# Kernel tuning notes

Hardware: AMD Instinct MI355X
Metric: run time of the kernel (lower is better)

## Reference

```python
import jax, jax.numpy as jnp
import numpy as np

B, T, E, H, M2 = 8, 2048, 256, 2, 134
HD = E // H


def setup_inputs() -> dict:
    key = jax.random.key(0)
    ks = jax.random.split(key, 10)
    s = 0.02
    return {
        "X": jax.random.normal(ks[0], (B, T, E), dtype=jnp.float32),
        "Y": jax.random.uniform(ks[1], (B, M2), dtype=jnp.float32),
        "wpe": s * jax.random.normal(ks[2], (T, E), dtype=jnp.float32),
        "ln1_g": jnp.ones((E,), jnp.float32), "ln1_b": jnp.zeros((E,), jnp.float32),
        "attn_w": s * jax.random.normal(ks[3], (3 * E, E), dtype=jnp.float32),
        "attn_b": jnp.zeros((3 * E,), jnp.float32),
        "attnproj_w": s * jax.random.normal(ks[4], (E, E), dtype=jnp.float32),
        "attnproj_b": jnp.zeros((E,), jnp.float32),
        "ln2_g": jnp.ones((E,), jnp.float32), "ln2_b": jnp.zeros((E,), jnp.float32),
        "fc_w": s * jax.random.normal(ks[5], (2 * E, E), dtype=jnp.float32),
        "fc_b": jnp.zeros((2 * E,), jnp.float32),
        "mlpproj_w": s * jax.random.normal(ks[6], (E, 2 * E), dtype=jnp.float32),
        "mlpproj_b": jnp.zeros((E,), jnp.float32),
        "lnf_g": jnp.ones((E,), jnp.float32), "lnf_b": jnp.zeros((E,), jnp.float32),
        "head_w": s * jax.random.normal(ks[7], (M2, E), dtype=jnp.float32),
        "head_b": jnp.zeros((M2,), jnp.float32),
    }


def _ln(x, g, b, eps=1e-5):
    mu = x.mean(-1, keepdims=True)
    var = ((x - mu) ** 2).mean(-1, keepdims=True)
    return (x - mu) * jax.lax.rsqrt(var + eps) * g + b


def reference(X, Y, wpe, ln1_g, ln1_b, attn_w, attn_b, attnproj_w, attnproj_b,
              ln2_g, ln2_b, fc_w, fc_b, mlpproj_w, mlpproj_b, lnf_g, lnf_b,
              head_w, head_b):
    # positional ids = arange(T) -> wpe itself; cls ids = [0]*T/2 + [1]*T/2
    cls_ids = np.concatenate([np.zeros(T // 2, np.int32), np.ones(T // 2, np.int32)])
    x = X + wpe + wpe[cls_ids]                      # [B,T,E] (dropout = identity, eval)

    # single Block (n_layer=1), preceded by ReLU as in cross_mod loop
    x = jax.nn.relu(x)
    h = _ln(x, ln1_g, ln1_b)
    qkv = h @ attn_w.T + attn_b                     # [B,T,3E]
    q, k, v = jnp.split(qkv, 3, axis=-1)
    q, k, v = jax.nn.relu(q), jax.nn.relu(k), jax.nn.relu(v)
    split_heads = lambda t: t.reshape(B, T, H, HD).transpose(0, 2, 1, 3)
    q, k, v = split_heads(q), split_heads(k), split_heads(v)
    att = jnp.einsum('bhqd,bhkd->bhqk', q, k) * (1.0 / np.sqrt(HD))
    tril = jnp.tril(jnp.ones((T, T), dtype=bool))
    # masked_fill(-inf) then ReLU  ==  zero outside causal mask, ReLU inside
    att = jnp.where(tril, jax.nn.relu(att), 0.0)    # [B,H,T,T]
    y = jnp.einsum('bhqk,bhkd->bhqd', att, v)
    y = y.transpose(0, 2, 1, 3).reshape(B, T, E)
    x = x + (y @ attnproj_w.T + attnproj_b)

    h = _ln(x, ln2_g, ln2_b)
    x = x + (jax.nn.relu(h @ fc_w.T + fc_b) @ mlpproj_w.T + mlpproj_b)

    x = jax.nn.relu(x)
    x = _ln(x, lnf_g, lnf_b)
    x = jax.nn.relu(x)
    emb = x.mean(axis=1)                            # [B,E]
    logits = jax.nn.relu(emb @ head_w.T + head_b)   # [B,M2]

    loss1 = jnp.sqrt(jnp.mean((logits - Y) ** 2))
    e1, e2 = emb[:, : E // 2], emb[:, E // 2:]
    loss3 = jnp.sqrt(jnp.mean((e1 - e2) ** 2))
    loss = 50.0 * loss1 + loss3
    return (e1, e2, loss, loss1, loss3, logits)
```

## Files before the change

### kernel.cpp

```cpp
#include <hip/hip_runtime.h>
#include <hip/hip_bf16.h>

#define Bc 8
#define Tc 2048
#define Ec 256
#define Hc 2
#define HDc 128
#define Mrows (Bc*Tc)
#define M2c 134

using bfx8  = __attribute__((ext_vector_type(8))) __bf16;
using f32x4 = __attribute__((ext_vector_type(4))) float;

__device__ __forceinline__ void gll16(const __bf16* g, __bf16* lds) {
    __builtin_amdgcn_global_load_lds(
        (const __attribute__((address_space(1))) unsigned int*)g,
        (__attribute__((address_space(3))) unsigned int*)lds, 16, 0, 0);
}

__global__ __launch_bounds__(256) void embed_prep_k(const float* X, const float* wpe,
                                                    const float* g, const float* bb,
                                                    const float* attn_w, const float* apw,
                                                    const float* fcw, const float* mpw,
                                                    __bf16* wb, float* embsum,
                                                    __bf16* xres, __bf16* hb) {
    int m = blockIdx.x;
    int e = threadIdx.x;
    if (m < 2048) {
        int i = m * 256 + e;
        if (i < 196608)       wb[i] = (__bf16)attn_w[i];
        else if (i < 262144)  wb[i] = (__bf16)apw[i - 196608];
        else if (i < 393216)  wb[i] = (__bf16)fcw[i - 262144];
        else                  wb[i] = (__bf16)mpw[i - 393216];
        if (m < 8) embsum[m * 256 + e] = 0.f;
    }
    int t = m & (Tc - 1);
    float v = X[(size_t)m * Ec + e] + wpe[(size_t)t * Ec + e] + wpe[(size_t)(t >= 1024) * Ec + e];
    v = fmaxf(v, 0.f);
    xres[(size_t)m * Ec + e] = (__bf16)v;
    float s1 = v, s2 = v * v;
    #pragma unroll
    for (int o = 32; o; o >>= 1) { s1 += __shfl_xor(s1, o, 64); s2 += __shfl_xor(s2, o, 64); }
    __shared__ float a1[4], a2[4];
    int w = threadIdx.x >> 6;
    if ((threadIdx.x & 63) == 0) { a1[w] = s1; a2[w] = s2; }
    __syncthreads();
    float m1 = (a1[0] + a1[1] + a1[2] + a1[3]) * (1.f / 256.f);
    float m2 = (a2[0] + a2[1] + a2[2] + a2[3]) * (1.f / 256.f);
    float r = rsqrtf(m2 - m1 * m1 + 1e-5f);
    hb[(size_t)m * Ec + e] = (__bf16)((v - m1) * r * g[e] + bb[e]);
}

__global__ __launch_bounds__(256) void gemm_qkv(const __bf16* __restrict__ A,
                                                const __bf16* __restrict__ Bw,
                                                const float* __restrict__ bias,
                                                __bf16* __restrict__ Qb,
                                                __bf16* __restrict__ Kb,
                                                __bf16* __restrict__ Vb) {
    const int K = 256;
    __shared__ __bf16 As[128 * 64];
    __shared__ __bf16 Bs[128 * 64];
    const int tid = threadIdx.x, w = tid >> 6, l = tid & 63;
    const int m0 = blockIdx.y * 128, n0 = blockIdx.x * 128;
    const int wr = w >> 1, wc = w & 1;
    const int quad = l >> 4, col15 = l & 15;

    f32x4 acc[4][4];
    f32x4 zz = {0.f, 0.f, 0.f, 0.f};
    #pragma unroll
    for (int i = 0; i < 4; i++)
        #pragma unroll
        for (int j = 0; j < 4; j++) acc[i][j] = zz;

    const int lrow = l >> 3;
    const int pbs  = l & 7;

    for (int kb = 0; kb < K; kb += 64) {
        #pragma unroll
        for (int it = 0; it < 4; it++) {
            int chunk = w * 4 + it;
            int row = chunk * 8 + lrow;
            int lb = pbs ^ (row & 7);
            gll16(A  + (size_t)(m0 + row) * K + kb + lb * 8, As + chunk * 512);
            gll16(Bw + (size_t)(n0 + row) * K + kb + lb * 8, Bs + chunk * 512);
        }
        __syncthreads();
        #pragma unroll
        for (int ks = 0; ks < 2; ks++) {
            bfx8 af[4], bfr[4];
            #pragma unroll
            for (int rt = 0; rt < 4; rt++) {
                int row = wr * 64 + rt * 16 + col15;
                int pb = (ks * 4 + quad) ^ (row & 7);
                af[rt] = *(const bfx8*)(As + row * 64 + pb * 8);
            }
            #pragma unroll
            for (int ct = 0; ct < 4; ct++) {
                int row = wc * 64 + ct * 16 + col15;
                int pb = (ks * 4 + quad) ^ (row & 7);
                bfr[ct] = *(const bfx8*)(Bs + row * 64 + pb * 8);
            }
            #pragma unroll
            for (int rt = 0; rt < 4; rt++)
                #pragma unroll
                for (int ct = 0; ct < 4; ct++)
                    acc[rt][ct] = __builtin_amdgcn_mfma_f32_16x16x32_bf16(af[rt], bfr[ct], acc[rt][ct], 0, 0, 0);
        }
        __syncthreads();
    }

    #pragma unroll
    for (int rt = 0; rt < 4; rt++)
        #pragma unroll
        for (int ct = 0; ct < 4; ct++) {
            int mgb = m0 + wr * 64 + rt * 16 + quad * 4;
            int ng  = n0 + wc * 64 + ct * 16 + col15;
            float bsv = bias[ng];
            #pragma unroll
            for (int r = 0; r < 4; r++) {
                float val = fmaxf(acc[rt][ct][r] + bsv, 0.f);
                int mg = mgb + r;
                int sel = ng >> 8;
                int hh = (ng >> 7) & 1;
                int d = ng & 127;
                int bb = mg >> 11, tt = mg & (Tc - 1);
                size_t idx = ((size_t)((bb * 2 + hh) * Tc + tt)) * HDc + d;
                __bf16 bv = (__bf16)val;
                if (sel == 0) Qb[idx] = bv;
                else if (sel == 1) Kb[idx] = bv;
                else Vb[idx] = bv;
            }
        }
}

__global__ __launch_bounds__(256) void transpose_v(const unsigned short* Vb, unsigned short* Vt) {
    __shared__ unsigned short tile[64][66];
    int kt = blockIdx.x, dt = blockIdx.y, bh = blockIdx.z;
    int tid = threadIdx.x;
    int k0 = kt * 64, d0 = dt * 64;
    int rr = tid >> 4, cc = (tid & 15) * 4;
    #pragma unroll
    for (int p = 0; p < 4; p++) {
        int k = p * 16 + rr;
        const unsigned short* src = Vb + ((size_t)(bh * Tc + k0 + k)) * HDc + d0 + cc;
        ushort4 vv = *(const ushort4*)src;
        tile[k][cc] = vv.x; tile[k][cc + 1] = vv.y; tile[k][cc + 2] = vv.z; tile[k][cc + 3] = vv.w;
    }
    __syncthreads();
    #pragma unroll
    for (int p = 0; p < 4; p++) {
        int d = p * 16 + rr;
        unsigned short* dst = Vt + ((size_t)(bh * HDc + d0 + d)) * Tc + k0 + cc;
        ushort4 ov;
        ov.x = tile[cc][d]; ov.y = tile[cc + 1][d]; ov.z = tile[cc + 2][d]; ov.w = tile[cc + 3][d];
        *(ushort4*)dst = ov;
    }
}

__global__ __launch_bounds__(256, 4) void attn6_k(const __bf16* __restrict__ Qb,
                                                  const __bf16* __restrict__ Kb,
                                                  const __bf16* __restrict__ Vt,
                                                  __bf16* __restrict__ Y1,
                                                  __bf16* __restrict__ Y2,
                                                  __bf16* __restrict__ Y3,
                                                  __bf16* __restrict__ Y4) {
    __shared__ __bf16 Ks[64 * 128];
    __shared__ __bf16 Vs[128 * 64];
    __shared__ __bf16 Ss[64 * 64];
    int bid = blockIdx.x;
    int lane8 = bid & 7;
    int s = bid >> 3;
    int bh = ((s & 1) << 3) | lane8;
    int f = s >> 1;
    int qt, ch;
    if (f < 8)       { qt = f;                    ch = 0; }
    else if (f < 24) { qt = 8 + ((f - 8) >> 1);   ch = (f - 8) & 1; }
    else if (f < 48) { int r = f - 24; int d3 = r / 3; qt = 16 + d3; ch = r - 3 * d3; }
    else             { int r = f - 48; qt = 24 + (r >> 2); ch = r & 3; }
    int Q0 = qt * 64;
    int kts = ch * 8;
    int kte = min(kts + 8, qt + 1);

    int tid = threadIdx.x, w = tid >> 6, l = tid & 63;
    int quad = l >> 4, col15 = l & 15;
    const int lrowK = l >> 4, pbsK = l & 15;
    const int lrowV = l >> 3, pbsV = l & 7;

    #pragma unroll
    for (int it = 0; it < 4; it++) {
        int chunk = w * 4 + it;
        int row = chunk * 4 + lrowK;
        int lb = pbsK ^ (row & 7);
        gll16(Qb + ((size_t)(bh * Tc + Q0 + row)) * HDc + lb * 8, Ks + chunk * 512);
    }
    __syncthreads();
    bfx8 qf[4];
    #pragma unroll
    for (int ks = 0; ks < 4; ks++) {
        int row = w * 16 + col15;
        int pb = (ks * 4 + quad) ^ (row & 7);
        qf[ks] = *(const bfx8*)(Ks + row * 128 + pb * 8);
    }

    f32x4 zz = {0.f, 0.f, 0.f, 0.f};
    f32x4 yacc[8];
    #pragma unroll
    for (int i = 0; i < 8; i++) yacc[i] = zz;

    for (int kt = kts; kt < kte; kt++) {
        __syncthreads();
        #pragma unroll
        for (int it = 0; it < 4; it++) {
            int chunk = w * 4 + it;
            int rowK = chunk * 4 + lrowK;
            int lbK = pbsK ^ (rowK & 7);
            gll16(Kb + ((size_t)(bh * Tc + kt * 64 + rowK)) * HDc + lbK * 8, Ks + chunk * 512);
            int rowV = chunk * 8 + lrowV;
            int lbV = pbsV ^ (rowV & 7);
            gll16(Vt + ((size_t)(bh * HDc + rowV)) * Tc + kt * 64 + lbV * 8, Vs + chunk * 512);
        }
        __syncthreads();

        f32x4 sacc[4];
        #pragma unroll
        for (int i = 0; i < 4; i++) sacc[i] = zz;
        #pragma unroll
        for (int ks = 0; ks < 4; ks++) {
            #pragma unroll
            for (int ct = 0; ct < 4; ct++) {
                int row = ct * 16 + col15;
                int pb = (ks * 4 + quad) ^ (row & 7);
                bfx8 kf = *(const bfx8*)(Ks + row * 128 + pb * 8);
                sacc[ct] = __builtin_amdgcn_mfma_f32_16x16x32_bf16(qf[ks], kf, sacc[ct], 0, 0, 0);
            }
        }

        #pragma unroll
        for (int ct = 0; ct < 4; ct++) {
            int kl = ct * 16 + col15;
            int kg = kt * 64 + kl;
            int blk = kl >> 3, off = kl & 7;
            #pragma unroll
            for (int r = 0; r < 4; r++) {
                int qlw = w * 16 + quad * 4 + r;
                float val = (kg <= Q0 + qlw) ? fmaxf(sacc[ct][r], 0.f) : 0.f;
                int pb = blk ^ (qlw & 7);
                Ss[qlw * 64 + pb * 8 + off] = (__bf16)val;
            }
        }

        #pragma unroll
        for (int ks = 0; ks < 2; ks++) {
            int rowS = w * 16 + col15;
            int pbS = (ks * 4 + quad) ^ (rowS & 7);
            bfx8 sf = *(const bfx8*)(Ss + rowS * 64 + pbS * 8);
            #pragma unroll
            for (int dt = 0; dt < 8; dt++) {
                int row = dt * 16 + col15;
                int pb = (ks * 4 + quad) ^ (row & 7);
                bfx8 vf = *(const bfx8*)(Vs + row * 64 + pb * 8);
                yacc[dt] = __builtin_amdgcn_mfma_f32_16x16x32_bf16(sf, vf, yacc[dt], 0, 0, 0);
            }
        }
    }

    __bf16* Yp = (ch == 0) ? Y1 : (ch == 1) ? Y2 : (ch == 2) ? Y3 : Y4;
    int b = bh >> 1, h = bh & 1;
    const float sc = 0.08838834764831845f;
    #pragma unroll
    for (int dt = 0; dt < 8; dt++) {
        int d = dt * 16 + col15;
        #pragma unroll
        for (int r = 0; r < 4; r++) {
            int q = Q0 + w * 16 + quad * 4 + r;
            Yp[((size_t)(b * Tc + q)) * Ec + h * HDc + d] = (__bf16)(yacc[dt][r] * sc);
        }
    }
}

__global__ __launch_bounds__(256, 1) void mega_k(const __bf16* __restrict__ Y1,
                                                 const __bf16* __restrict__ Y2,
                                                 const __bf16* __restrict__ Y3,
                                                 const __bf16* __restrict__ Y4,
                                                 const __bf16* __restrict__ wap,
                                                 const float* __restrict__ apb,
                                                 const __bf16* __restrict__ xres,
                                                 const float* __restrict__ ln2_g,
                                                 const float* __restrict__ ln2_b,
                                                 const __bf16* __restrict__ wfc,
                                                 const float* __restrict__ fcb,
                                                 const __bf16* __restrict__ wmp,
                                                 const float* __restrict__ mpb,
                                                 const float* __restrict__ lnf_g,
                                                 const float* __restrict__ lnf_b,
                                                 float* __restrict__ embsum) {
    __shared__ __bf16 h2s[4 * 4096];
    __shared__ __bf16 fc64[8 * 4096];
    __shared__ __bf16 Bs[256 * 64];
    __shared__ float cs[256];
    const int tid = threadIdx.x, w = tid >> 6, l = tid & 63;
    const int m0 = blockIdx.x * 64;
    const int quad = l >> 4, col15 = l & 15;
    const int lrow = l >> 3, pbs = l & 7;
    f32x4 zz = {0.f, 0.f, 0.f, 0.f};
    cs[tid] = 0.f;

    int nsum = (((m0 & (Tc - 1)) >> 6) + 8) >> 3;
    const __bf16* Ys[4] = {Y1, Y2, Y3, Y4};
    __bf16* As = fc64;

    f32x4 acc[16];
    #pragma unroll
    for (int i = 0; i < 16; i++) acc[i] = zz;

    for (int kb = 0; kb < 256; kb += 64) {
        bfx8 av[2]; int rows[2], blks[2];
        #pragma unroll
        for (int it = 0; it < 2; it++) {
            int idx = it * 256 + tid;
            int row = idx >> 3, blk = idx & 7;
            rows[it] = row; blks[it] = blk;
            size_t off = (size_t)(m0 + row) * 256 + kb + blk * 8;
            bfx8 a1 = *(const bfx8*)(Y1 + off);
            float tmp[8];
            #pragma unroll
            for (int jj = 0; jj < 8; jj++) tmp[jj] = (float)a1[jj];
            for (int j = 1; j < nsum; j++) {
                bfx8 aj = *(const bfx8*)(Ys[j] + off);
                #pragma unroll
                for (int jj = 0; jj < 8; jj++) tmp[jj] += (float)aj[jj];
            }
            #pragma unroll
            for (int jj = 0; jj < 8; jj++) a1[jj] = (__bf16)tmp[jj];
            av[it] = a1;
        }
        __syncthreads();
        #pragma unroll
        for (int it = 0; it < 2; it++) {
            int row = rows[it];
            int pb = blks[it] ^ (row & 7);
            *(bfx8*)(As + row * 64 + pb * 8) = av[it];
        }
        #pragma unroll
        for (int it = 0; it < 8; it++) {
            int chunk = w * 8 + it;
            int row = chunk * 8 + lrow;
            int lb = pbs ^ (row & 7);
            gll16(wap + (size_t)row * 256 + kb + lb * 8, Bs + chunk * 512);
        }
        __syncthreads();
        #pragma unroll
        for (int ks = 0; ks < 2; ks++) {
            int arow = w * 16 + col15;
            int apbk = (ks * 4 + quad) ^ (arow & 7);
            bfx8 af = *(const bfx8*)(As + arow * 64 + apbk * 8);
            #pragma unroll
            for (int ct = 0; ct < 16; ct++) {
                int brow = ct * 16 + col15;
                int bpb = (ks * 4 + quad) ^ (brow & 7);
                bfx8 bf = *(const bfx8*)(Bs + brow * 64 + bpb * 8);
                acc[ct] = __builtin_amdgcn_mfma_f32_16x16x32_bf16(af, bf, acc[ct], 0, 0, 0);
            }
        }
    }

    float xv[16][4];
    #pragma unroll
    for (int ct = 0; ct < 16; ct++) {
        int ng = ct * 16 + col15;
        float bsv = apb[ng];
        #pragma unroll
        for (int r = 0; r < 4; r++) {
            int mg = m0 + w * 16 + quad * 4 + r;
            xv[ct][r] = acc[ct][r] + bsv + (float)xres[(size_t)mg * 256 + ng];
        }
    }
    {
        float s1[4], s2[4];
        #pragma unroll
        for (int r = 0; r < 4; r++) {
            float a = 0.f, b2 = 0.f;
            #pragma unroll
            for (int ct = 0; ct < 16; ct++) { a += xv[ct][r]; b2 += xv[ct][r] * xv[ct][r]; }
            #pragma unroll
            for (int o = 1; o < 16; o <<= 1) { a += __shfl_xor(a, o, 64); b2 += __shfl_xor(b2, o, 64); }
            s1[r] = a; s2[r] = b2;
        }
        #pragma unroll
        for (int r = 0; r < 4; r++) {
            float mu = s1[r] * (1.f / 256.f);
            float var = s2[r] * (1.f / 256.f) - mu * mu;
            float rs = rsqrtf(var + 1e-5f);
            int row = w * 16 + quad * 4 + r;
            #pragma unroll
            for (int ct = 0; ct < 16; ct++) {
                int ng = ct * 16 + col15;
                float h = (xv[ct][r] - mu) * rs * ln2_g[ng] + ln2_b[ng];
                int panel = ng >> 6, c = ng & 63;
                h2s[panel * 4096 + row * 64 + ((c >> 3) ^ (row & 7)) * 8 + (c & 7)] = (__bf16)h;
            }
        }
    }

    for (int half = 0; half < 2; half++) {
        f32x4 acc2[16];
        #pragma unroll
        for (int i = 0; i < 16; i++) acc2[i] = zz;
        for (int kb = 0; kb < 256; kb += 64) {
            __syncthreads();
            #pragma unroll
            for (int it = 0; it < 8; it++) {
                int chunk = w * 8 + it;
                int row = chunk * 8 + lrow;
                int lb = pbs ^ (row & 7);
                gll16(wfc + (size_t)(half * 256 + row) * 256 + kb + lb * 8, Bs + chunk * 512);
            }
            __syncthreads();
            int panel = kb >> 6;
            #pragma unroll
            for (int ks = 0; ks < 2; ks++) {
                int arow = w * 16 + col15;
                int apbk = (ks * 4 + quad) ^ (arow & 7);
                bfx8 af = *(const bfx8*)(h2s + panel * 4096 + arow * 64 + apbk * 8);
                #pragma unroll
                for (int ct = 0; ct < 16; ct++) {
                    int brow = ct * 16 + col15;
                    int bpb = (ks * 4 + quad) ^ (brow & 7);
                    bfx8 bf = *(const bfx8*)(Bs + brow * 64 + bpb * 8);
                    acc2[ct] = __builtin_amdgcn_mfma_f32_16x16x32_bf16(af, bf, acc2[ct], 0, 0, 0);
                }
            }
        }
        #pragma unroll
        for (int ct = 0; ct < 16; ct++) {
            int col = half * 256 + ct * 16 + col15;
            float bsv = fcb[col];
            int panel = col >> 6, c = col & 63;
            #pragma unroll
            for (int r = 0; r < 4; r++) {
                int row = w * 16 + quad * 4 + r;
                float val = fmaxf(acc2[ct][r] + bsv, 0.f);
                fc64[panel * 4096 + row * 64 + ((c >> 3) ^ (row & 7)) * 8 + (c & 7)] = (__bf16)val;
            }
        }
    }

    #pragma unroll
    for (int i = 0; i < 16; i++) acc[i] = zz;
    for (int kb = 0; kb < 512; kb += 64) {
        __syncthreads();
        #pragma unroll
        for (int it = 0; it < 8; it++) {
            int chunk = w * 8 + it;
            int row = chunk * 8 + lrow;
            int lb = pbs ^ (row & 7);
            gll16(wmp + (size_t)row * 512 + kb + lb * 8, Bs + chunk * 512);
        }
        __syncthreads();
        int panel = kb >> 6;
        #pragma unroll
        for (int ks = 0; ks < 2; ks++) {
            int arow = w * 16 + col15;
            int apbk = (ks * 4 + quad) ^ (arow & 7);
            bfx8 af = *(const bfx8*)(fc64 + panel * 4096 + arow * 64 + apbk * 8);
            #pragma unroll
            for (int ct = 0; ct < 16; ct++) {
                int brow = ct * 16 + col15;
                int bpb = (ks * 4 + quad) ^ (brow & 7);
                bfx8 bf = *(const bfx8*)(Bs + brow * 64 + bpb * 8);
                acc[ct] = __builtin_amdgcn_mfma_f32_16x16x32_bf16(af, bf, acc[ct], 0, 0, 0);
            }
        }
    }

    #pragma unroll
    for (int ct = 0; ct < 16; ct++) {
        int ng = ct * 16 + col15;
        float bsv = mpb[ng];
        #pragma unroll
        for (int r = 0; r < 4; r++)
            xv[ct][r] = fmaxf(acc[ct][r] + bsv + xv[ct][r], 0.f);
    }
    float s1[4], s2[4];
    #pragma unroll
    for (int r = 0; r < 4; r++) {
        float a = 0.f, b2 = 0.f;
        #pragma unroll
        for (int ct = 0; ct < 16; ct++) { a += xv[ct][r]; b2 += xv[ct][r] * xv[ct][r]; }
        #pragma unroll
        for (int o = 1; o < 16; o <<= 1) { a += __shfl_xor(a, o, 64); b2 += __shfl_xor(b2, o, 64); }
        s1[r] = a; s2[r] = b2;
    }
    float colsum[16];
    #pragma unroll
    for (int ct = 0; ct < 16; ct++) colsum[ct] = 0.f;
    #pragma unroll
    for (int r = 0; r < 4; r++) {
        float mu = s1[r] * (1.f / 256.f);
        float var = s2[r] * (1.f / 256.f) - mu * mu;
        float rs = rsqrtf(var + 1e-5f);
        #pragma unroll
        for (int ct = 0; ct < 16; ct++) {
            int ng = ct * 16 + col15;
            float h = (xv[ct][r] - mu) * rs * lnf_g[ng] + lnf_b[ng];
            colsum[ct] += fmaxf(h, 0.f);
        }
    }
    #pragma unroll
    for (int ct = 0; ct < 16; ct++) {
        colsum[ct] += __shfl_xor(colsum[ct], 16, 64);
        colsum[ct] += __shfl_xor(colsum[ct], 32, 64);
    }
    if (quad == 0) {
        #pragma unroll
        for (int ct = 0; ct < 16; ct++)
            atomicAdd(&cs[ct * 16 + col15], colsum[ct]);
    }
    __syncthreads();
    atomicAdd(&embsum[(m0 >> 11) * 256 + tid], cs[tid]);
}

__global__ __launch_bounds__(256) void final_k(const float* embsum, const float* Yt,
                                               const float* head_w, const float* head_b,
                                               float* out) {
    __shared__ float semb[2048];
    __shared__ float slog[1072];
    int tid = threadIdx.x;
    for (int i = tid; i < 2048; i += 256) semb[i] = embsum[i] * (1.f / 2048.f);
    __syncthreads();
    float part1 = 0.f;
    for (int idx = tid; idx < 1072; idx += 256) {
        int b = idx / M2c, n = idx - b * M2c;
        float acc = head_b[n];
        const float* wn = head_w + (size_t)n * Ec;
        const float* e = semb + b * Ec;
        #pragma unroll 8
        for (int k = 0; k < Ec; k++) acc += e[k] * wn[k];
        acc = fmaxf(acc, 0.f);
        slog[idx] = acc;
        float d = acc - Yt[idx];
        part1 += d * d;
    }
    float part3 = 0.f;
    for (int idx = tid; idx < 1024; idx += 256) {
        int b = idx >> 7, i = idx & 127;
        float d = semb[b * Ec + i] - semb[b * Ec + 128 + i];
        part3 += d * d;
    }
    #pragma unroll
    for (int o = 32; o; o >>= 1) { part1 += __shfl_xor(part1, o, 64); part3 += __shfl_xor(part3, o, 64); }
    __shared__ float r1[4], r3[4];
    int w = tid >> 6;
    if ((tid & 63) == 0) { r1[w] = part1; r3[w] = part3; }
    __syncthreads();
    float l1 = sqrtf((r1[0] + r1[1] + r1[2] + r1[3]) / 1072.f);
    float l3 = sqrtf((r3[0] + r3[1] + r3[2] + r3[3]) / 1024.f);
    for (int idx = tid; idx < 1024; idx += 256) {
        int b = idx >> 7, i = idx & 127;
        out[idx]        = semb[b * Ec + i];
        out[1024 + idx] = semb[b * Ec + 128 + i];
    }
    if (tid == 0) {
        out[2048] = 50.f * l1 + l3;
        out[2049] = l1;
        out[2050] = l3;
    }
    for (int idx = tid; idx < 1072; idx += 256) out[2051 + idx] = slog[idx];
}

extern "C" void kernel_launch(void* const* d_in, const int* in_sizes, int n_in,
                              void* d_out, int out_size, void* d_ws, size_t ws_size,
                              hipStream_t stream) {
    const float* X        = (const float*)d_in[0];
    const float* Yt       = (const float*)d_in[1];
    const float* wpe      = (const float*)d_in[2];
    const float* ln1_g    = (const float*)d_in[3];
    const float* ln1_b    = (const float*)d_in[4];
    const float* attn_w   = (const float*)d_in[5];
    const float* attn_b   = (const float*)d_in[6];
    const float* apw      = (const float*)d_in[7];
    const float* apb      = (const float*)d_in[8];
    const float* ln2_g    = (const float*)d_in[9];
    const float* ln2_b    = (const float*)d_in[10];
    const float* fcw      = (const float*)d_in[11];
    const float* fcb      = (const float*)d_in[12];
    const float* mpw      = (const float*)d_in[13];
    const float* mpb      = (const float*)d_in[14];
    const float* lnf_g    = (const float*)d_in[15];
    const float* lnf_b    = (const float*)d_in[16];
    const float* head_w   = (const float*)d_in[17];
    const float* head_b   = (const float*)d_in[18];

    char* ws = (char*)d_ws;
    const size_t MB = 1048576;
    __bf16* xres   = (__bf16*)(ws + 0 * MB);
    __bf16* hb     = (__bf16*)(ws + 8 * MB);
    __bf16* Qb     = (__bf16*)(ws + 16 * MB);
    __bf16* Kb     = (__bf16*)(ws + 24 * MB);
    __bf16* Vb     = (__bf16*)(ws + 32 * MB);
    __bf16* Vt     = (__bf16*)(ws + 40 * MB);
    __bf16* Y1     = (__bf16*)(ws + 48 * MB);
    __bf16* Y2     = (__bf16*)(ws + 56 * MB);
    __bf16* wb     = (__bf16*)(ws + 64 * MB);
    float*  embsum = (float*)(ws + 65 * MB);

    __bf16* Y3 = hb;
    __bf16* Y4 = Vb;

    __bf16* wqkv = wb;
    __bf16* wap  = wb + 196608;
    __bf16* wfc  = wb + 262144;
    __bf16* wmp  = wb + 393216;

    embed_prep_k<<<Mrows, 256, 0, stream>>>(X, wpe, ln1_g, ln1_b,
                                            attn_w, apw, fcw, mpw, wb, embsum, xres, hb);
    gemm_qkv<<<dim3(6, 128), 256, 0, stream>>>(hb, wqkv, attn_b, Qb, Kb, Vb);
    transpose_v<<<dim3(32, 2, 16), 256, 0, stream>>>((const unsigned short*)Vb, (unsigned short*)Vt);
    attn6_k<<<1280, 256, 0, stream>>>(Qb, Kb, Vt, Y1, Y2, Y3, Y4);
    mega_k<<<256, 256, 0, stream>>>(Y1, Y2, Y3, Y4, wap, apb, xres, ln2_g, ln2_b,
                                    wfc, fcb, wmp, mpb, lnf_g, lnf_b, embsum);
    final_k<<<1, 256, 0, stream>>>(embsum, Yt, head_w, head_b, (float*)d_out);
}
```

Before: 250.4 us.

## Fuse V transpose into QKV GEMM epilogue and pair causal query tiles in attention

The QKV GEMM now writes V already transposed via an LDS staging tile, so the separate transpose kernel and its extra global round trip are gone. The attention kernel pairs query tile p with tile 31-p so every block gets equal causal work split into four chunks, sharing each K/V tile load between both query tiles. The mega kernel now always sums all four partial outputs. In exchange, attention uses more registers and LDS (occupancy hint lowered to 3) and the GEMM gains a 34KB transpose buffer, which may lower its occupancy.

```diff
diff --git a/kernel.cpp b/kernel.cpp
--- a/kernel.cpp
+++ b/kernel.cpp
@@ -56,14 +56,16 @@
                                                 const float* __restrict__ bias,
                                                 __bf16* __restrict__ Qb,
                                                 __bf16* __restrict__ Kb,
-                                                __bf16* __restrict__ Vb) {
+                                                unsigned short* __restrict__ Vt) {
     const int K = 256;
     __shared__ __bf16 As[128 * 64];
     __shared__ __bf16 Bs[128 * 64];
+    __shared__ unsigned short trans[128][136];
     const int tid = threadIdx.x, w = tid >> 6, l = tid & 63;
     const int m0 = blockIdx.y * 128, n0 = blockIdx.x * 128;
     const int wr = w >> 1, wc = w & 1;
     const int quad = l >> 4, col15 = l & 15;
+    const int isV = (n0 >= 512);
 
     f32x4 acc[4][4];
     f32x4 zz = {0.f, 0.f, 0.f, 0.f};
@@ -113,51 +115,43 @@
     for (int rt = 0; rt < 4; rt++)
         #pragma unroll
         for (int ct = 0; ct < 4; ct++) {
-            int mgb = m0 + wr * 64 + rt * 16 + quad * 4;
             int ng  = n0 + wc * 64 + ct * 16 + col15;
             float bsv = bias[ng];
             #pragma unroll
             for (int r = 0; r < 4; r++) {
+                int mg = m0 + wr * 64 + rt * 16 + quad * 4 + r;
                 float val = fmaxf(acc[rt][ct][r] + bsv, 0.f);
-                int mg = mgb + r;
-                int sel = ng >> 8;
-                int hh = (ng >> 7) & 1;
-                int d = ng & 127;
-                int bb = mg >> 11, tt = mg & (Tc - 1);
-                size_t idx = ((size_t)((bb * 2 + hh) * Tc + tt)) * HDc + d;
                 __bf16 bv = (__bf16)val;
-                if (sel == 0) Qb[idx] = bv;
-                else if (sel == 1) Kb[idx] = bv;
-                else Vb[idx] = bv;
-            }
-        }
+                if (isV) {
+                    int d = ng & 127;
+                    int tl = mg - m0;
+                    trans[d][tl] = *(unsigned short*)&bv;
+                } else {
+                    int sel = ng >> 8;
+                    int hh = (ng >> 7) & 1;
+                    int d = ng & 127;
+                    int bb = mg >> 11, tt = mg & (Tc - 1);
+                    size_t idx = ((size_t)((bb * 2 + hh) * Tc + tt)) * HDc + d;
+                    if (sel == 0) Qb[idx] = bv;
+                    else Kb[idx] = bv;
+                }
+            }
+        }
+    if (isV) {
+        __syncthreads();
+        int h = (n0 >> 7) & 1;
+        int b = m0 >> 11, t0 = m0 & (Tc - 1);
+        int bh = b * 2 + h;
+        int d = tid >> 1, th = tid & 1;
+        unsigned short* dst = Vt + ((size_t)(bh * HDc + d)) * Tc + t0 + th * 64;
+        const unsigned short* src = &trans[d][th * 64];
+        #pragma unroll
+        for (int i = 0; i < 8; i++)
+            *(uint4*)(dst + i * 8) = *(const uint4*)(src + i * 8);
+    }
 }
 
-__global__ __launch_bounds__(256) void transpose_v(const unsigned short* Vb, unsigned short* Vt) {
-    __shared__ unsigned short tile[64][66];
-    int kt = blockIdx.x, dt = blockIdx.y, bh = blockIdx.z;
-    int tid = threadIdx.x;
-    int k0 = kt * 64, d0 = dt * 64;
-    int rr = tid >> 4, cc = (tid & 15) * 4;
-    #pragma unroll
-    for (int p = 0; p < 4; p++) {
-        int k = p * 16 + rr;
-        const unsigned short* src = Vb + ((size_t)(bh * Tc + k0 + k)) * HDc + d0 + cc;
-        ushort4 vv = *(const ushort4*)src;
-        tile[k][cc] = vv.x; tile[k][cc + 1] = vv.y; tile[k][cc + 2] = vv.z; tile[k][cc + 3] = vv.w;
-    }
-    __syncthreads();
-    #pragma unroll
-    for (int p = 0; p < 4; p++) {
-        int d = p * 16 + rr;
-        unsigned short* dst = Vt + ((size_t)(bh * HDc + d0 + d)) * Tc + k0 + cc;
-        ushort4 ov;
-        ov.x = tile[cc][d]; ov.y = tile[cc + 1][d]; ov.z = tile[cc + 2][d]; ov.w = tile[cc + 3][d];
-        *(ushort4*)dst = ov;
-    }
-}
-
-__global__ __launch_bounds__(256, 4) void attn6_k(const __bf16* __restrict__ Qb,
+__global__ __launch_bounds__(256, 3) void attn7_k(const __bf16* __restrict__ Qb,
                                                   const __bf16* __restrict__ Kb,
                                                   const __bf16* __restrict__ Vt,
                                                   __bf16* __restrict__ Y1,
@@ -166,48 +160,69 @@
                                                   __bf16* __restrict__ Y4) {
     __shared__ __bf16 Ks[64 * 128];
     __shared__ __bf16 Vs[128 * 64];
-    __shared__ __bf16 Ss[64 * 64];
+    __shared__ __bf16 SsA[64 * 64];
+    __shared__ __bf16 SsB[64 * 64];
     int bid = blockIdx.x;
     int lane8 = bid & 7;
     int s = bid >> 3;
     int bh = ((s & 1) << 3) | lane8;
     int f = s >> 1;
-    int qt, ch;
-    if (f < 8)       { qt = f;                    ch = 0; }
-    else if (f < 24) { qt = 8 + ((f - 8) >> 1);   ch = (f - 8) & 1; }
-    else if (f < 48) { int r = f - 24; int d3 = r / 3; qt = 16 + d3; ch = r - 3 * d3; }
-    else             { int r = f - 48; qt = 24 + (r >> 2); ch = r & 3; }
-    int Q0 = qt * 64;
-    int kts = ch * 8;
-    int kte = min(kts + 8, qt + 1);
+    int p = f >> 2, ch = f & 3;
+    int Q0A = p * 64, Q0B = (31 - p) * 64;
+    const int offs[5] = {0, 9, 17, 25, 33};
+    int u0 = offs[ch], u1 = offs[ch + 1];
+    int twoP = 2 * (p + 1);
 
     int tid = threadIdx.x, w = tid >> 6, l = tid & 63;
     int quad = l >> 4, col15 = l & 15;
     const int lrowK = l >> 4, pbsK = l & 15;
     const int lrowV = l >> 3, pbsV = l & 7;
 
+    bfx8 qfA[4], qfB[4];
     #pragma unroll
     for (int it = 0; it < 4; it++) {
         int chunk = w * 4 + it;
         int row = chunk * 4 + lrowK;
         int lb = pbsK ^ (row & 7);
-        gll16(Qb + ((size_t)(bh * Tc + Q0 + row)) * HDc + lb * 8, Ks + chunk * 512);
+        gll16(Qb + ((size_t)(bh * Tc + Q0A + row)) * HDc + lb * 8, Ks + chunk * 512);
     }
     __syncthreads();
-    bfx8 qf[4];
     #pragma unroll
     for (int ks = 0; ks < 4; ks++) {
         int row = w * 16 + col15;
         int pb = (ks * 4 + quad) ^ (row & 7);
-        qf[ks] = *(const bfx8*)(Ks + row * 128 + pb * 8);
+        qfA[ks] = *(const bfx8*)(Ks + row * 128 + pb * 8);
+    }
+    __syncthreads();
+    #pragma unroll
+    for (int it = 0; it < 4; it++) {
+        int chunk = w * 4 + it;
+        int row = chunk * 4 + lrowK;
+        int lb = pbsK ^ (row & 7);
+        gll16(Qb + ((size_t)(bh * Tc + Q0B + row)) * HDc + lb * 8, Ks + chunk * 512);
+    }
+    __syncthreads();
+    #pragma unroll
+    for (int ks = 0; ks < 4; ks++) {
+        int row = w * 16 + col15;
+        int pb = (ks * 4 + quad) ^ (row & 7);
+        qfB[ks] = *(const bfx8*)(Ks + row * 128 + pb * 8);
     }
 
     f32x4 zz = {0.f, 0.f, 0.f, 0.f};
-    f32x4 yacc[8];
-    #pragma unroll
-    for (int i = 0; i < 8; i++) yacc[i] = zz;
-
-    for (int kt = kts; kt < kte; kt++) {
+    f32x4 yaccA[8], yaccB[8];
+    #pragma unroll
+    for (int i = 0; i < 8; i++) { yaccA[i] = zz; yaccB[i] = zz; }
+
+    int u = u0;
+    while (u < u1) {
+        int kt, hasA, hasB;
+        if (u < twoP) {
+            kt = u >> 1;
+            if ((u & 1) == 0) { hasA = 1; hasB = (u + 1 < u1) ? 1 : 0; u += 1 + hasB; }
+            else              { hasA = 0; hasB = 1; u += 1; }
+        } else { kt = u - p - 1; hasA = 0; hasB = 1; u += 1; }
+
         __syncthreads();
         #pragma unroll
         for (int it = 0; it < 4; it++) {
@@ -221,17 +236,27 @@
         }
         __syncthreads();
 
-        f32x4 sacc[4];
-        #pragma unroll
-        for (int i = 0; i < 4; i++) sacc[i] = zz;
+        f32x4 sA[4], sB[4];
+        #pragma unroll
+        for (int i = 0; i < 4; i++) { sA[i] = zz; sB[i] = zz; }
         #pragma unroll
         for (int ks = 0; ks < 4; ks++) {
+            bfx8 kf[4];
             #pragma unroll
             for (int ct = 0; ct < 4; ct++) {
                 int row = ct * 16 + col15;
                 int pb = (ks * 4 + quad) ^ (row & 7);
-                bfx8 kf = *(const bfx8*)(Ks + row * 128 + pb * 8);
-                sacc[ct] = __builtin_amdgcn_mfma_f32_16x16x32_bf16(qf[ks], kf, sacc[ct], 0, 0, 0);
+                kf[ct] = *(const bfx8*)(Ks + row * 128 + pb * 8);
+            }
+            if (hasB) {
+                #pragma unroll
+                for (int ct = 0; ct < 4; ct++)
+                    sB[ct] = __builtin_amdgcn_mfma_f32_16x16x32_bf16(qfB[ks], kf[ct], sB[ct], 0, 0, 0);
+            }
+            if (hasA) {
+                #pragma unroll
+                for (int ct = 0; ct < 4; ct++)
+                    sA[ct] = __builtin_amdgcn_mfma_f32_16x16x32_bf16(qfA[ks], kf[ct], sA[ct], 0, 0, 0);
             }
         }
 
@@ -243,9 +268,15 @@
             #pragma unroll
             for (int r = 0; r < 4; r++) {
                 int qlw = w * 16 + quad * 4 + r;
-                float val = (kg <= Q0 + qlw) ? fmaxf(sacc[ct][r], 0.f) : 0.f;
                 int pb = blk ^ (qlw & 7);
-                Ss[qlw * 64 + pb * 8 + off] = (__bf16)val;
+                if (hasB) {
+                    float vB = (kg <= Q0B + qlw) ? fmaxf(sB[ct][r], 0.f) : 0.f;
+                    SsB[qlw * 64 + pb * 8 + off] = (__bf16)vB;
+                }
+                if (hasA) {
+                    float vA = (kg <= Q0A + qlw) ? fmaxf(sA[ct][r], 0.f) : 0.f;
+                    SsA[qlw * 64 + pb * 8 + off] = (__bf16)vA;
+                }
             }
         }
 
@@ -253,13 +284,16 @@
         for (int ks = 0; ks < 2; ks++) {
             int rowS = w * 16 + col15;
             int pbS = (ks * 4 + quad) ^ (rowS & 7);
-            bfx8 sf = *(const bfx8*)(Ss + rowS * 64 + pbS * 8);
+            bfx8 sfB, sfA;
+            if (hasB) sfB = *(const bfx8*)(SsB + rowS * 64 + pbS * 8);
+            if (hasA) sfA = *(const bfx8*)(SsA + rowS * 64 + pbS * 8);
             #pragma unroll
             for (int dt = 0; dt < 8; dt++) {
                 int row = dt * 16 + col15;
                 int pb = (ks * 4 + quad) ^ (row & 7);
                 bfx8 vf = *(const bfx8*)(Vs + row * 64 + pb * 8);
-                yacc[dt] = __builtin_amdgcn_mfma_f32_16x16x32_bf16(sf, vf, yacc[dt], 0, 0, 0);
+                if (hasB) yaccB[dt] = __builtin_amdgcn_mfma_f32_16x16x32_bf16(sfB, vf, yaccB[dt], 0, 0, 0);
+                if (hasA) yaccA[dt] = __builtin_amdgcn_mfma_f32_16x16x32_bf16(sfA, vf, yaccA[dt], 0, 0, 0);
             }
         }
     }
@@ -272,8 +306,10 @@
         int d = dt * 16 + col15;
         #pragma unroll
         for (int r = 0; r < 4; r++) {
-            int q = Q0 + w * 16 + quad * 4 + r;
-            Yp[((size_t)(b * Tc + q)) * Ec + h * HDc + d] = (__bf16)(yacc[dt][r] * sc);
+            int qa = Q0A + w * 16 + quad * 4 + r;
+            int qb2 = Q0B + w * 16 + quad * 4 + r;
+            Yp[((size_t)(b * Tc + qa)) * Ec + h * HDc + d] = (__bf16)(yaccA[dt][r] * sc);
+            Yp[((size_t)(b * Tc + qb2)) * Ec + h * HDc + d] = (__bf16)(yaccB[dt][r] * sc);
         }
     }
 }
@@ -304,9 +340,6 @@
     const int lrow = l >> 3, pbs = l & 7;
     f32x4 zz = {0.f, 0.f, 0.f, 0.f};
     cs[tid] = 0.f;
-
-    int nsum = (((m0 & (Tc - 1)) >> 6) + 8) >> 3;
-    const __bf16* Ys[4] = {Y1, Y2, Y3, Y4};
     __bf16* As = fc64;
 
     f32x4 acc[16];
@@ -322,16 +355,12 @@
             rows[it] = row; blks[it] = blk;
             size_t off = (size_t)(m0 + row) * 256 + kb + blk * 8;
             bfx8 a1 = *(const bfx8*)(Y1 + off);
-            float tmp[8];
-            #pragma unroll
-            for (int jj = 0; jj < 8; jj++) tmp[jj] = (float)a1[jj];
-            for (int j = 1; j < nsum; j++) {
-                bfx8 aj = *(const bfx8*)(Ys[j] + off);
-                #pragma unroll
-                for (int jj = 0; jj < 8; jj++) tmp[jj] += (float)aj[jj];
-            }
-            #pragma unroll
-            for (int jj = 0; jj < 8; jj++) a1[jj] = (__bf16)tmp[jj];
+            bfx8 a2 = *(const bfx8*)(Y2 + off);
+            bfx8 a3 = *(const bfx8*)(Y3 + off);
+            bfx8 a4 = *(const bfx8*)(Y4 + off);
+            #pragma unroll
+            for (int jj = 0; jj < 8; jj++)
+                a1[jj] = (__bf16)(((float)a1[jj] + (float)a2[jj]) + ((float)a3[jj] + (float)a4[jj]));
             av[it] = a1;
         }
         __syncthreads();
@@ -614,9 +643,8 @@
 
     embed_prep_k<<<Mrows, 256, 0, stream>>>(X, wpe, ln1_g, ln1_b,
                                             attn_w, apw, fcw, mpw, wb, embsum, xres, hb);
-    gemm_qkv<<<dim3(6, 128), 256, 0, stream>>>(hb, wqkv, attn_b, Qb, Kb, Vb);
-    transpose_v<<<dim3(32, 2, 16), 256, 0, stream>>>((const unsigned short*)Vb, (unsigned short*)Vt);
-    attn6_k<<<1280, 256, 0, stream>>>(Qb, Kb, Vt, Y1, Y2, Y3, Y4);
+    gemm_qkv<<<dim3(6, 128), 256, 0, stream>>>(hb, wqkv, attn_b, Qb, Kb, (unsigned short*)Vt);
+    attn7_k<<<1024, 256, 0, stream>>>(Qb, Kb, Vt, Y1, Y2, Y3, Y4);
     mega_k<<<256, 256, 0, stream>>>(Y1, Y2, Y3, Y4, wap, apb, xres, ln2_g, ln2_b,
                                     wfc, fcb, wmp, mpb, lnf_g, lnf_b, embsum);
     final_k<<<1, 256, 0, stream>>>(embsum, Yt, head_w, head_b, (float*)d_out);
```

Result: slower. 373.9 us (+49.3%).

## Fuse V transpose into QKV GEMM epilogue and use 128-row query tiles

Applied to the files above, without the earlier changes.

The QKV GEMM now writes V directly in transposed layout through an LDS staging tile, which removes the separate transpose kernel and its extra round trip through global memory. The attention kernel moves from 64-row to 128-row query tiles, with each wave handling two 16-row subtiles. This reuses each K/V tile load across twice as many queries and halves the grid. The costs are more registers and LDS per block (occupancy hint lowered from 4 to 3) and a larger LDS footprint in the GEMM. The chunk-count formula in mega_k is updated to match the new split.

```diff
diff --git a/kernel.cpp b/kernel.cpp
--- a/kernel.cpp
+++ b/kernel.cpp
@@ -56,14 +56,16 @@
                                                 const float* __restrict__ bias,
                                                 __bf16* __restrict__ Qb,
                                                 __bf16* __restrict__ Kb,
-                                                __bf16* __restrict__ Vb) {
+                                                unsigned short* __restrict__ Vt) {
     const int K = 256;
     __shared__ __bf16 As[128 * 64];
     __shared__ __bf16 Bs[128 * 64];
+    __shared__ unsigned short trans[128][136];
     const int tid = threadIdx.x, w = tid >> 6, l = tid & 63;
     const int m0 = blockIdx.y * 128, n0 = blockIdx.x * 128;
     const int wr = w >> 1, wc = w & 1;
     const int quad = l >> 4, col15 = l & 15;
+    const int isV = (n0 >= 512);
 
     f32x4 acc[4][4];
     f32x4 zz = {0.f, 0.f, 0.f, 0.f};
@@ -113,73 +115,66 @@
     for (int rt = 0; rt < 4; rt++)
         #pragma unroll
         for (int ct = 0; ct < 4; ct++) {
-            int mgb = m0 + wr * 64 + rt * 16 + quad * 4;
             int ng  = n0 + wc * 64 + ct * 16 + col15;
             float bsv = bias[ng];
             #pragma unroll
             for (int r = 0; r < 4; r++) {
+                int mg = m0 + wr * 64 + rt * 16 + quad * 4 + r;
                 float val = fmaxf(acc[rt][ct][r] + bsv, 0.f);
-                int mg = mgb + r;
-                int sel = ng >> 8;
-                int hh = (ng >> 7) & 1;
-                int d = ng & 127;
-                int bb = mg >> 11, tt = mg & (Tc - 1);
-                size_t idx = ((size_t)((bb * 2 + hh) * Tc + tt)) * HDc + d;
                 __bf16 bv = (__bf16)val;
-                if (sel == 0) Qb[idx] = bv;
-                else if (sel == 1) Kb[idx] = bv;
-                else Vb[idx] = bv;
-            }
-        }
+                if (isV) {
+                    int d = ng & 127;
+                    int tl = mg - m0;
+                    trans[d][tl] = *(unsigned short*)&bv;
+                } else {
+                    int sel = ng >> 8;
+                    int hh = (ng >> 7) & 1;
+                    int d = ng & 127;
+                    int bb = mg >> 11, tt = mg & (Tc - 1);
+                    size_t idx = ((size_t)((bb * 2 + hh) * Tc + tt)) * HDc + d;
+                    if (sel == 0) Qb[idx] = bv;
+                    else Kb[idx] = bv;
+                }
+            }
+        }
+    if (isV) {
+        __syncthreads();
+        int h = (n0 >> 7) & 1;
+        int b = m0 >> 11, t0 = m0 & (Tc - 1);
+        int bh = b * 2 + h;
+        int d = tid >> 1, th = tid & 1;
+        unsigned short* dst = Vt + ((size_t)(bh * HDc + d)) * Tc + t0 + th * 64;
+        const unsigned short* src = &trans[d][th * 64];
+        #pragma unroll
+        for (int i = 0; i < 8; i++)
+            *(uint4*)(dst + i * 8) = *(const uint4*)(src + i * 8);
+    }
 }
 
-__global__ __launch_bounds__(256) void transpose_v(const unsigned short* Vb, unsigned short* Vt) {
-    __shared__ unsigned short tile[64][66];
-    int kt = blockIdx.x, dt = blockIdx.y, bh = blockIdx.z;
-    int tid = threadIdx.x;
-    int k0 = kt * 64, d0 = dt * 64;
-    int rr = tid >> 4, cc = (tid & 15) * 4;
-    #pragma unroll
-    for (int p = 0; p < 4; p++) {
-        int k = p * 16 + rr;
-        const unsigned short* src = Vb + ((size_t)(bh * Tc + k0 + k)) * HDc + d0 + cc;
-        ushort4 vv = *(const ushort4*)src;
-        tile[k][cc] = vv.x; tile[k][cc + 1] = vv.y; tile[k][cc + 2] = vv.z; tile[k][cc + 3] = vv.w;
-    }
-    __syncthreads();
-    #pragma unroll
-    for (int p = 0; p < 4; p++) {
-        int d = p * 16 + rr;
-        unsigned short* dst = Vt + ((size_t)(bh * HDc + d0 + d)) * Tc + k0 + cc;
-        ushort4 ov;
-        ov.x = tile[cc][d]; ov.y = tile[cc + 1][d]; ov.z = tile[cc + 2][d]; ov.w = tile[cc + 3][d];
-        *(ushort4*)dst = ov;
-    }
-}
-
-__global__ __launch_bounds__(256, 4) void attn6_k(const __bf16* __restrict__ Qb,
+__global__ __launch_bounds__(256, 3) void attn8_k(const __bf16* __restrict__ Qb,
                                                   const __bf16* __restrict__ Kb,
                                                   const __bf16* __restrict__ Vt,
                                                   __bf16* __restrict__ Y1,
                                                   __bf16* __restrict__ Y2,
                                                   __bf16* __restrict__ Y3,
                                                   __bf16* __restrict__ Y4) {
-    __shared__ __bf16 Ks[64 * 128];
-    __shared__ __bf16 Vs[128 * 64];
-    __shared__ __bf16 Ss[64 * 64];
+    __shared__ __bf16 smem[3 * 8192];
+    __bf16* Ks = smem;
+    __bf16* Vs = smem + 8192;
+    __bf16* Ss = smem + 16384;
     int bid = blockIdx.x;
     int lane8 = bid & 7;
     int s = bid >> 3;
     int bh = ((s & 1) << 3) | lane8;
     int f = s >> 1;
     int qt, ch;
-    if (f < 8)       { qt = f;                    ch = 0; }
-    else if (f < 24) { qt = 8 + ((f - 8) >> 1);   ch = (f - 8) & 1; }
-    else if (f < 48) { int r = f - 24; int d3 = r / 3; qt = 16 + d3; ch = r - 3 * d3; }
-    else             { int r = f - 48; qt = 24 + (r >> 2); ch = r & 3; }
-    int Q0 = qt * 64;
+    if (f < 4)       { qt = f;                   ch = 0; }
+    else if (f < 12) { qt = 4 + ((f - 4) >> 1);  ch = (f - 4) & 1; }
+    else if (f < 24) { int r = f - 12; int d3 = r / 3; qt = 8 + d3; ch = r - 3 * d3; }
+    else             { int r = f - 24; qt = 12 + (r >> 2); ch = r & 3; }
+    int Q0 = qt * 128;
     int kts = ch * 8;
-    int kte = min(kts + 8, qt + 1);
+    int kte = min(kts + 8, 2 * qt + 2);
 
     int tid = threadIdx.x, w = tid >> 6, l = tid & 63;
     int quad = l >> 4, col15 = l & 15;
@@ -187,25 +182,29 @@
     const int lrowV = l >> 3, pbsV = l & 7;
 
     #pragma unroll
-    for (int it = 0; it < 4; it++) {
-        int chunk = w * 4 + it;
+    for (int it = 0; it < 8; it++) {
+        int chunk = w * 8 + it;
         int row = chunk * 4 + lrowK;
         int lb = pbsK ^ (row & 7);
-        gll16(Qb + ((size_t)(bh * Tc + Q0 + row)) * HDc + lb * 8, Ks + chunk * 512);
+        gll16(Qb + ((size_t)(bh * Tc + Q0 + row)) * HDc + lb * 8, smem + chunk * 512);
     }
     __syncthreads();
-    bfx8 qf[4];
-    #pragma unroll
-    for (int ks = 0; ks < 4; ks++) {
-        int row = w * 16 + col15;
-        int pb = (ks * 4 + quad) ^ (row & 7);
-        qf[ks] = *(const bfx8*)(Ks + row * 128 + pb * 8);
-    }
+    bfx8 qf[2][4];
+    #pragma unroll
+    for (int rt = 0; rt < 2; rt++)
+        #pragma unroll
+        for (int ks = 0; ks < 4; ks++) {
+            int row = w * 32 + rt * 16 + col15;
+            int pb = (ks * 4 + quad) ^ (row & 7);
+            qf[rt][ks] = *(const bfx8*)(smem + row * 128 + pb * 8);
+        }
 
     f32x4 zz = {0.f, 0.f, 0.f, 0.f};
-    f32x4 yacc[8];
-    #pragma unroll
-    for (int i = 0; i < 8; i++) yacc[i] = zz;
+    f32x4 yacc[2][8];
+    #pragma unroll
+    for (int rt = 0; rt < 2; rt++)
+        #pragma unroll
+        for (int i = 0; i < 8; i++) yacc[rt][i] = zz;
 
     for (int kt = kts; kt < kte; kt++) {
         __syncthreads();
@@ -221,45 +220,60 @@
         }
         __syncthreads();
 
-        f32x4 sacc[4];
-        #pragma unroll
-        for (int i = 0; i < 4; i++) sacc[i] = zz;
+        f32x4 sacc[2][4];
+        #pragma unroll
+        for (int rt = 0; rt < 2; rt++)
+            #pragma unroll
+            for (int i = 0; i < 4; i++) sacc[rt][i] = zz;
         #pragma unroll
         for (int ks = 0; ks < 4; ks++) {
+            bfx8 kf[4];
             #pragma unroll
             for (int ct = 0; ct < 4; ct++) {
                 int row = ct * 16 + col15;
                 int pb = (ks * 4 + quad) ^ (row & 7);
-                bfx8 kf = *(const bfx8*)(Ks + row * 128 + pb * 8);
-                sacc[ct] = __builtin_amdgcn_mfma_f32_16x16x32_bf16(qf[ks], kf, sacc[ct], 0, 0, 0);
-            }
-        }
-
-        #pragma unroll
-        for (int ct = 0; ct < 4; ct++) {
-            int kl = ct * 16 + col15;
-            int kg = kt * 64 + kl;
-            int blk = kl >> 3, off = kl & 7;
-            #pragma unroll
-            for (int r = 0; r < 4; r++) {
-                int qlw = w * 16 + quad * 4 + r;
-                float val = (kg <= Q0 + qlw) ? fmaxf(sacc[ct][r], 0.f) : 0.f;
-                int pb = blk ^ (qlw & 7);
-                Ss[qlw * 64 + pb * 8 + off] = (__bf16)val;
-            }
-        }
+                kf[ct] = *(const bfx8*)(Ks + row * 128 + pb * 8);
+            }
+            #pragma unroll
+            for (int rt = 0; rt < 2; rt++)
+                #pragma unroll
+                for (int ct = 0; ct < 4; ct++)
+                    sacc[rt][ct] = __builtin_amdgcn_mfma_f32_16x16x32_bf16(qf[rt][ks], kf[ct], sacc[rt][ct], 0, 0, 0);
+        }
+
+        #pragma unroll
+        for (int rt = 0; rt < 2; rt++)
+            #pragma unroll
+            for (int ct = 0; ct < 4; ct++) {
+                int kl = ct * 16 + col15;
+                int kg = kt * 64 + kl;
+                int blk = kl >> 3, off = kl & 7;
+                #pragma unroll
+                for (int r = 0; r < 4; r++) {
+                    int qlw = w * 32 + rt * 16 + quad * 4 + r;
+                    float val = (kg <= Q0 + qlw) ? fmaxf(sacc[rt][ct][r], 0.f) : 0.f;
+                    int pb = blk ^ (qlw & 7);
+                    Ss[qlw * 64 + pb * 8 + off] = (__bf16)val;
+                }
+            }
 
         #pragma unroll
         for (int ks = 0; ks < 2; ks++) {
-            int rowS = w * 16 + col15;
-            int pbS = (ks * 4 + quad) ^ (rowS & 7);
-            bfx8 sf = *(const bfx8*)(Ss + rowS * 64 + pbS * 8);
+            bfx8 sf[2];
+            #pragma unroll
+            for (int rt = 0; rt < 2; rt++) {
+                int rowS = w * 32 + rt * 16 + col15;
+                int pbS = (ks * 4 + quad) ^ (rowS & 7);
+                sf[rt] = *(const bfx8*)(Ss + rowS * 64 + pbS * 8);
+            }
             #pragma unroll
             for (int dt = 0; dt < 8; dt++) {
                 int row = dt * 16 + col15;
                 int pb = (ks * 4 + quad) ^ (row & 7);
                 bfx8 vf = *(const bfx8*)(Vs + row * 64 + pb * 8);
-                yacc[dt] = __builtin_amdgcn_mfma_f32_16x16x32_bf16(sf, vf, yacc[dt], 0, 0, 0);
+                #pragma unroll
+                for (int rt = 0; rt < 2; rt++)
+                    yacc[rt][dt] = __builtin_amdgcn_mfma_f32_16x16x32_bf16(sf[rt], vf, yacc[rt][dt], 0, 0, 0);
             }
         }
     }
@@ -268,14 +282,16 @@
     int b = bh >> 1, h = bh & 1;
     const float sc = 0.08838834764831845f;
     #pragma unroll
-    for (int dt = 0; dt < 8; dt++) {
-        int d = dt * 16 + col15;
-        #pragma unroll
-        for (int r = 0; r < 4; r++) {
-            int q = Q0 + w * 16 + quad * 4 + r;
-            Yp[((size_t)(b * Tc + q)) * Ec + h * HDc + d] = (__bf16)(yacc[dt][r] * sc);
-        }
-    }
+    for (int rt = 0; rt < 2; rt++)
+        #pragma unroll
+        for (int dt = 0; dt < 8; dt++) {
+            int d = dt * 16 + col15;
+            #pragma unroll
+            for (int r = 0; r < 4; r++) {
+                int q = Q0 + w * 32 + rt * 16 + quad * 4 + r;
+                Yp[((size_t)(b * Tc + q)) * Ec + h * HDc + d] = (__bf16)(yacc[rt][dt][r] * sc);
+            }
+        }
 }
 
 __global__ __launch_bounds__(256, 1) void mega_k(const __bf16* __restrict__ Y1,
@@ -304,10 +320,11 @@
     const int lrow = l >> 3, pbs = l & 7;
     f32x4 zz = {0.f, 0.f, 0.f, 0.f};
     cs[tid] = 0.f;
-
-    int nsum = (((m0 & (Tc - 1)) >> 6) + 8) >> 3;
+    __bf16* As = fc64;
+
+    int qt128 = (m0 & (Tc - 1)) >> 7;
+    int nsum = (2 * qt128 + 9) >> 3;
     const __bf16* Ys[4] = {Y1, Y2, Y3, Y4};
-    __bf16* As = fc64;
 
     f32x4 acc[16];
     #pragma unroll
@@ -614,9 +631,8 @@
 
     embed_prep_k<<<Mrows, 256, 0, stream>>>(X, wpe, ln1_g, ln1_b,
                                             attn_w, apw, fcw, mpw, wb, embsum, xres, hb);
-    gemm_qkv<<<dim3(6, 128), 256, 0, stream>>>(hb, wqkv, attn_b, Qb, Kb, Vb);
-    transpose_v<<<dim3(32, 2, 16), 256, 0, stream>>>((const unsigned short*)Vb, (unsigned short*)Vt);
-    attn6_k<<<1280, 256, 0, stream>>>(Qb, Kb, Vt, Y1, Y2, Y3, Y4);
+    gemm_qkv<<<dim3(6, 128), 256, 0, stream>>>(hb, wqkv, attn_b, Qb, Kb, (unsigned short*)Vt);
+    attn8_k<<<640, 256, 0, stream>>>(Qb, Kb, Vt, Y1, Y2, Y3, Y4);
     mega_k<<<256, 256, 0, stream>>>(Y1, Y2, Y3, Y4, wap, apb, xres, ln2_g, ln2_b,
                                     wfc, fcb, wmp, mpb, lnf_g, lnf_b, embsum);
     final_k<<<1, 256, 0, stream>>>(embsum, Yt, head_w, head_b, (float*)d_out);
```

Result: slower. 331.7 us (+32.5%).
